# Kernel tuning notes

Hardware: AMD Instinct MI355X
Metric: run time of the kernel (lower is better)

## Reference

```python
import jax, jax.numpy as jnp
import numpy as np

EPS = 1e-8      # laplace_transform epsilon
RC = 0.5        # residual_coff
L = 2           # num_layers
NU, NB, NI, D = 100000, 30000, 50000, 128
E_UB, E_UI, E_BI = 300000, 500000, 500000


def _l2norm(x):
    # F.normalize(x, p=2, dim=1)
    n = jnp.linalg.norm(x, axis=1, keepdims=True)
    return x / jnp.maximum(n, 1e-12)


def _spmm(rows, cols, vals, feats, n):
    # sparse (COO) matmul: out[r] += vals[e] * feats[cols[e]]
    return jax.ops.segment_sum(vals[:, None] * feats[cols], rows, num_segments=n)


def _sym_norm_graph(u, v, na, nb):
    # bipartite block matrix [[0, B],[B^T, 0]] with D^-1/2 A D^-1/2 normalization
    rows = jnp.concatenate([u, v + na])
    cols = jnp.concatenate([v + na, u])
    deg = jax.ops.segment_sum(jnp.ones(rows.shape[0], jnp.float32), rows,
                              num_segments=na + nb)
    dinv = 1.0 / (jnp.sqrt(deg) + EPS)
    vals = dinv[rows] * dinv[cols]
    return rows, cols, vals


def _one_propagate(rows, cols, vals, afeat, bfeat):
    n = afeat.shape[0] + bfeat.shape[0]
    feats = jnp.concatenate([afeat, bfeat], axis=0)
    ini = _l2norm(feats)
    acc = feats  # all_feats starts with raw feats, summed at the end
    for i in range(L):
        feats = _spmm(rows, cols, vals, feats, n)
        feats = (feats + RC * ini) / (i + 2)
        feats = _l2norm(feats)
        acc = acc + feats
    return acc[:afeat.shape[0]], acc[afeat.shape[0]:]


def setup_inputs() -> dict:
    key = jax.random.key(0)
    ks = jax.random.split(key, 10)
    return {
        "users_feat": jax.random.normal(ks[0], (NU, D), jnp.float32) * 0.1,
        "bundles_feat": jax.random.normal(ks[1], (NB, D), jnp.float32) * 0.1,
        "items_feat": jax.random.normal(ks[2], (NI, D), jnp.float32) * 0.1,
        "bi_vals": jax.random.uniform(ks[3], (E_BI,), jnp.float32),
        "ub_u": jax.random.randint(ks[4], (E_UB,), 0, NU),
        "ub_b": jax.random.randint(ks[5], (E_UB,), 0, NB),
        "ui_u": jax.random.randint(ks[6], (E_UI,), 0, NU),
        "ui_i": jax.random.randint(ks[7], (E_UI,), 0, NI),
        "bi_b": jax.random.randint(ks[8], (E_BI,), 0, NB),
        "bi_i": jax.random.randint(ks[9], (E_BI,), 0, NI),
    }


def reference(users_feat, bundles_feat, items_feat, bi_vals,
              ub_u, ub_b, ui_u, ui_i, bi_b, bi_i):
    nu, nb, ni = users_feat.shape[0], bundles_feat.shape[0], items_feat.shape[0]
    # UB (history) propagation
    r, c, v = _sym_norm_graph(ub_u, ub_b, nu, nb)
    hist_users, hist_bundles = _one_propagate(r, c, v, users_feat, bundles_feat)
    # UI (affinity) propagation
    r, c, v = _sym_norm_graph(ui_u, ui_i, nu, ni)
    aff_users, ui_items = _one_propagate(r, c, v, users_feat, items_feat)
    # BI aggregation: bundles x items sparse graph @ item features
    aff_bundles = _spmm(bi_b, bi_i, bi_vals, ui_items, nb)
    # concat [aff_users, hist_users, aff_bundles, hist_bundles] along rows
    return jnp.concatenate([aff_users, hist_users, aff_bundles, hist_bundles], axis=0)
```

## Files before the change

kernel.cpp:

```cpp
#include <hip/hip_runtime.h>

#define FD   128
#define FDH  64
#define EPSN 1e-8f
#define RCC  0.5f
#define SCAN_TPB 256
#define SCAN_ELEMS 1024

typedef unsigned int uint;

__device__ __forceinline__ float wave_sum(float x) {
#pragma unroll
    for (int off = 32; off > 0; off >>= 1) x += __shfl_xor(x, off);
    return x;
}

__device__ __forceinline__ uint packbf2(float a, float b) {
    uint ua = __float_as_uint(a); ua += 0x7fffu + ((ua >> 16) & 1u);
    uint ub = __float_as_uint(b); ub += 0x7fffu + ((ub >> 16) & 1u);
    return (ua >> 16) | (ub & 0xffff0000u);
}
__device__ __forceinline__ float2 unpackbf2(uint v) {
    return make_float2(__uint_as_float(v << 16), __uint_as_float(v & 0xffff0000u));
}

__global__ void passA(const int* __restrict__ ub_u, const int* __restrict__ ub_b,
                      const int* __restrict__ ui_u, const int* __restrict__ ui_i,
                      const int* __restrict__ bi_b, const int* __restrict__ bi_i,
                      const float* __restrict__ uf, const float* __restrict__ bf,
                      const float* __restrict__ itf,
                      int E_UB, int E_UI, int E_BI, int NU, int NB, int n1, int n2, int NT,
                      int nblk_edges,
                      int* __restrict__ head, int2* __restrict__ pairLL,
                      uint* __restrict__ fini16, float* __restrict__ normf) {
    if ((int)blockIdx.x < nblk_edges) {
        int e = blockIdx.x * blockDim.x + threadIdx.x;
        if (e < E_UB) {
            int a = ub_u[e], b = ub_b[e] + NU;
            int s0 = 2 * e;
            int p0 = atomicExch(&head[a], s0);
            int p1 = atomicExch(&head[b], s0 + 1);
            ((int4*)pairLL)[e] = make_int4(p0, b, p1, a);
        } else if (e < E_UB + E_UI) {
            int f = e - E_UB;
            int a = ui_u[f], bl = ui_i[f] + NU;
            int s0 = 2 * E_UB + 2 * f;
            int p0 = atomicExch(&head[n1 + a], s0);
            int p1 = atomicExch(&head[n1 + bl], s0 + 1);
            ((int4*)pairLL)[E_UB + f] = make_int4(p0, bl, p1, a);
        } else if (e < E_UB + E_UI + E_BI) {
            int g = e - E_UB - E_UI;
            int s = 2 * E_UB + 2 * E_UI + g;
            int p = atomicExch(&head[n1 + n2 + bi_b[g]], s);
            pairLL[s] = make_int2(p, bi_i[g]);
        }
    } else {
        int w = (((int)blockIdx.x - nblk_edges) * blockDim.x + threadIdx.x) >> 6;
        int lane = threadIdx.x & 63;
        if (w >= NT) return;
        const float* src = (w < NU) ? uf + (size_t)w * FD
                         : (w < NU + NB) ? bf + (size_t)(w - NU) * FD
                         : itf + (size_t)(w - NU - NB) * FD;
        float2 x = ((const float2*)src)[lane];
        float ss = wave_sum(x.x * x.x + x.y * x.y);
        float nrm = sqrtf(ss);
        float inv = 1.0f / fmaxf(nrm, 1e-12f);
        fini16[(size_t)w * FDH + lane] = packbf2(x.x * inv, x.y * inv);
        if (lane == 0) normf[w] = nrm;
    }
}

__global__ void passB(const int* __restrict__ head, const int2* __restrict__ pairLL,
                      int NN, int n1, int n2, int NU, int NB,
                      const float* __restrict__ normf,
                      int* __restrict__ deg, float* __restrict__ dinv,
                      float* __restrict__ scaled1) {
    int r = blockIdx.x * blockDim.x + threadIdx.x;
    if (r > NN) return;
    if (r == NN) { deg[NN] = 0; return; }
    int c = 0;
    int s = head[r];
    while (s >= 0) { c++; s = pairLL[s].x; }
    deg[r] = c;
    int n12 = n1 + n2;
    if (r < n12) {
        float dv = 1.0f / (sqrtf((float)c) + EPSN);
        dinv[r] = dv;
        int node = (r < n1) ? r : ((r - n1 < NU) ? (r - n1) : (r - n1 + NB));
        scaled1[r] = dv * normf[node];
    }
}

__global__ void scan_a(const int* __restrict__ in, int* __restrict__ out,
                       int* __restrict__ bsum, int nelem) {
    __shared__ int tsum[SCAN_TPB];
    int tid = threadIdx.x;
    int base = blockIdx.x * SCAN_ELEMS + tid * 4;
    int v0 = (base + 0 < nelem) ? in[base + 0] : 0;
    int v1 = (base + 1 < nelem) ? in[base + 1] : 0;
    int v2 = (base + 2 < nelem) ? in[base + 2] : 0;
    int v3 = (base + 3 < nelem) ? in[base + 3] : 0;
    int s = v0 + v1 + v2 + v3;
    tsum[tid] = s;
    __syncthreads();
    for (int off = 1; off < SCAN_TPB; off <<= 1) {
        int y = (tid >= off) ? tsum[tid - off] : 0;
        __syncthreads();
        tsum[tid] += y;
        __syncthreads();
    }
    int excl = tsum[tid] - s;
    if (tid == SCAN_TPB - 1) bsum[blockIdx.x] = tsum[SCAN_TPB - 1];
    if (base + 0 < nelem) out[base + 0] = excl;
    excl += v0;
    if (base + 1 < nelem) out[base + 1] = excl;
    excl += v1;
    if (base + 2 < nelem) out[base + 2] = excl;
    excl += v2;
    if (base + 3 < nelem) out[base + 3] = excl;
}

__global__ void scan_b(int* __restrict__ bsum, int nb) {
    __shared__ int sm[512];
    int tid = threadIdx.x;
    int v = (tid < nb) ? bsum[tid] : 0;
    sm[tid] = v;
    __syncthreads();
    for (int off = 1; off < 512; off <<= 1) {
        int y = (tid >= off) ? sm[tid - off] : 0;
        __syncthreads();
        sm[tid] += y;
        __syncthreads();
    }
    if (tid < nb) bsum[tid] = sm[tid] - v;
}

__global__ void scan_c(int* __restrict__ out, const int* __restrict__ bsum, int nelem) {
    int base = blockIdx.x * SCAN_ELEMS + threadIdx.x * 4;
    int add = bsum[blockIdx.x];
#pragma unroll
    for (int k = 0; k < 4; ++k)
        if (base + k < nelem) out[base + k] += add;
}

__global__ void passC(const int* __restrict__ head, const int2* __restrict__ pairLL,
                      const int* __restrict__ rowptr, const float* __restrict__ bi_vals,
                      int NN, int n12, int S1,
                      int* __restrict__ cols, float* __restrict__ wts) {
    int r = blockIdx.x * blockDim.x + threadIdx.x;
    if (r >= NN) return;
    int pos = rowptr[r];
    int s = head[r];
    if (r < n12) {
        while (s >= 0) { int2 p = pairLL[s]; cols[pos++] = p.y; s = p.x; }
    } else {
        while (s >= 0) {
            int2 p = pairLL[s];
            cols[pos] = p.y;
            wts[pos - S1] = bi_vals[s - S1];
            pos++; s = p.x;
        }
    }
}

__global__ void spmm_L1(const int* __restrict__ rowptr, const int* __restrict__ cols,
                        const float* __restrict__ dinv, const float* __restrict__ scaled1,
                        const float* __restrict__ normf, const uint* __restrict__ fini16,
                        uint* __restrict__ facc16, uint* __restrict__ fX16,
                        int n1, int NU, int NB, int n12) {
    int w = (blockIdx.x * blockDim.x + threadIdx.x) >> 6;
    int lane = threadIdx.x & 63;
    if (w >= n12) return;
    int s = rowptr[w], e = rowptr[w + 1];
    bool ui = (w >= n1);
    int sB = ui ? n1 : 0;
    int nAdd = ui ? NB : 0;
    int node = ui ? ((w - n1 < NU) ? (w - n1) : (w - n1 + NB)) : w;
    float dr = dinv[w];
    float ax = 0.0f, ay = 0.0f;
    int j = s;
    for (; j + 4 <= e; j += 4) {
        int c0 = cols[j], c1 = cols[j + 1], c2 = cols[j + 2], c3 = cols[j + 3];
        float w0 = scaled1[sB + c0], w1 = scaled1[sB + c1];
        float w2 = scaled1[sB + c2], w3 = scaled1[sB + c3];
        int m0 = c0 + ((c0 >= NU) ? nAdd : 0);
        int m1 = c1 + ((c1 >= NU) ? nAdd : 0);
        int m2 = c2 + ((c2 >= NU) ? nAdd : 0);
        int m3 = c3 + ((c3 >= NU) ? nAdd : 0);
        uint x0 = fini16[(size_t)m0 * FDH + lane];
        uint x1 = fini16[(size_t)m1 * FDH + lane];
        uint x2 = fini16[(size_t)m2 * FDH + lane];
        uint x3 = fini16[(size_t)m3 * FDH + lane];
        float2 f0 = unpackbf2(x0), f1 = unpackbf2(x1);
        float2 f2 = unpackbf2(x2), f3 = unpackbf2(x3);
        ax = fmaf(w0, f0.x, ax); ay = fmaf(w0, f0.y, ay);
        ax = fmaf(w1, f1.x, ax); ay = fmaf(w1, f1.y, ay);
        ax = fmaf(w2, f2.x, ax); ay = fmaf(w2, f2.y, ay);
        ax = fmaf(w3, f3.x, ax); ay = fmaf(w3, f3.y, ay);
    }
    for (; j < e; ++j) {
        int c0 = cols[j];
        float w0 = scaled1[sB + c0];
        int m0 = c0 + ((c0 >= NU) ? nAdd : 0);
        float2 f0 = unpackbf2(fini16[(size_t)m0 * FDH + lane]);
        ax = fmaf(w0, f0.x, ax); ay = fmaf(w0, f0.y, ay);
    }
    float2 i0 = unpackbf2(fini16[(size_t)node * FDH + lane]);
    float vx = (dr * ax + RCC * i0.x) * 0.5f;
    float vy = (dr * ay + RCC * i0.y) * 0.5f;
    float ss = wave_sum(vx * vx + vy * vy);
    float inv = 1.0f / fmaxf(sqrtf(ss), 1e-12f);
    vx *= inv; vy *= inv;
    float nr = normf[node];
    facc16[(size_t)w * FDH + lane] = packbf2(fmaf(i0.x, nr, vx), fmaf(i0.y, nr, vy));
    fX16[(size_t)w * FDH + lane] = packbf2(vx * dr, vy * dr);
}

__global__ void spmm_L2(const int* __restrict__ rowptr, const int* __restrict__ cols,
                        const float* __restrict__ dinv, const uint* __restrict__ fini16,
                        const uint* __restrict__ facc16, const uint* __restrict__ fX16,
                        uint* __restrict__ items16, float* __restrict__ outp,
                        int n1, int NU, int NB, int n12) {
    int w = (blockIdx.x * blockDim.x + threadIdx.x) >> 6;
    int lane = threadIdx.x & 63;
    if (w >= n12) return;
    int s = rowptr[w], e = rowptr[w + 1];
    bool ui = (w >= n1);
    int sB = ui ? n1 : 0;
    int node = ui ? ((w - n1 < NU) ? (w - n1) : (w - n1 + NB)) : w;
    float dr = dinv[w];
    float ax = 0.0f, ay = 0.0f;
    int j = s;
    for (; j + 4 <= e; j += 4) {
        int c0 = cols[j], c1 = cols[j + 1], c2 = cols[j + 2], c3 = cols[j + 3];
        uint x0 = fX16[(size_t)(sB + c0) * FDH + lane];
        uint x1 = fX16[(size_t)(sB + c1) * FDH + lane];
        uint x2 = fX16[(size_t)(sB + c2) * FDH + lane];
        uint x3 = fX16[(size_t)(sB + c3) * FDH + lane];
        float2 f0 = unpackbf2(x0), f1 = unpackbf2(x1);
        float2 f2 = unpackbf2(x2), f3 = unpackbf2(x3);
        ax += f0.x + f1.x + f2.x + f3.x;
        ay += f0.y + f1.y + f2.y + f3.y;
    }
    for (; j < e; ++j) {
        float2 f0 = unpackbf2(fX16[(size_t)(sB + cols[j]) * FDH + lane]);
        ax += f0.x; ay += f0.y;
    }
    float2 i0 = unpackbf2(fini16[(size_t)node * FDH + lane]);
    float vx = (dr * ax + RCC * i0.x) * (1.0f / 3.0f);
    float vy = (dr * ay + RCC * i0.y) * (1.0f / 3.0f);
    float ss = wave_sum(vx * vx + vy * vy);
    float inv = 1.0f / fmaxf(sqrtf(ss), 1e-12f);
    vx *= inv; vy *= inv;
    float2 a0 = unpackbf2(facc16[(size_t)w * FDH + lane]);
    float anx = a0.x + vx, any = a0.y + vy;
    if (!ui) {
        size_t dst = (w < NU) ? (size_t)(NU + w) : (size_t)(2 * NU + NB + (w - NU));
        ((float2*)(outp + dst * FD))[lane] = make_float2(anx, any);
    } else {
        int l = w - n1;
        if (l < NU) ((float2*)(outp + (size_t)l * FD))[lane] = make_float2(anx, any);
        else        items16[(size_t)(l - NU) * FDH + lane] = packbf2(anx, any);
    }
}

__global__ void bi_gather(const int* __restrict__ rowptr, const int* __restrict__ cols,
                          const float* __restrict__ wts, int S1,
                          const uint* __restrict__ items16,
                          float* __restrict__ outb, int nb) {
    int w = (blockIdx.x * blockDim.x + threadIdx.x) >> 6;
    int lane = threadIdx.x & 63;
    if (w >= nb) return;
    int s = rowptr[w], e = rowptr[w + 1];
    float ax = 0.0f, ay = 0.0f;
    int j = s;
    for (; j + 4 <= e; j += 4) {
        int c0 = cols[j], c1 = cols[j + 1], c2 = cols[j + 2], c3 = cols[j + 3];
        float w0 = wts[j - S1], w1 = wts[j + 1 - S1];
        float w2 = wts[j + 2 - S1], w3 = wts[j + 3 - S1];
        uint x0 = items16[(size_t)c0 * FDH + lane];
        uint x1 = items16[(size_t)c1 * FDH + lane];
        uint x2 = items16[(size_t)c2 * FDH + lane];
        uint x3 = items16[(size_t)c3 * FDH + lane];
        float2 f0 = unpackbf2(x0), f1 = unpackbf2(x1);
        float2 f2 = unpackbf2(x2), f3 = unpackbf2(x3);
        ax = fmaf(w0, f0.x, ax); ay = fmaf(w0, f0.y, ay);
        ax = fmaf(w1, f1.x, ax); ay = fmaf(w1, f1.y, ay);
        ax = fmaf(w2, f2.x, ax); ay = fmaf(w2, f2.y, ay);
        ax = fmaf(w3, f3.x, ax); ay = fmaf(w3, f3.y, ay);
    }
    for (; j < e; ++j) {
        float w0 = wts[j - S1];
        float2 f0 = unpackbf2(items16[(size_t)cols[j] * FDH + lane]);
        ax = fmaf(w0, f0.x, ax); ay = fmaf(w0, f0.y, ay);
    }
    ((float2*)(outb + (size_t)w * FD))[lane] = make_float2(ax, ay);
}

extern "C" void kernel_launch(void* const* d_in, const int* in_sizes, int n_in,
                              void* d_out, int out_size, void* d_ws, size_t ws_size,
                              hipStream_t stream) {
    const float* users   = (const float*)d_in[0];
    const float* bundles = (const float*)d_in[1];
    const float* items   = (const float*)d_in[2];
    const float* bi_vals = (const float*)d_in[3];
    const int* ub_u = (const int*)d_in[4];
    const int* ub_b = (const int*)d_in[5];
    const int* ui_u = (const int*)d_in[6];
    const int* ui_i = (const int*)d_in[7];
    const int* bi_b = (const int*)d_in[8];
    const int* bi_i = (const int*)d_in[9];

    const int NU = in_sizes[0] / FD;
    const int NB = in_sizes[1] / FD;
    const int NI = in_sizes[2] / FD;
    const int E_BI = in_sizes[3];
    const int E_UB = in_sizes[4];
    const int E_UI = in_sizes[6];
    float* out = (float*)d_out;

    const int n1 = NU + NB, n2 = NU + NI;
    const int n12 = n1 + n2;
    const int NT = NU + NB + NI;
    const int NN = n12 + NB;
    const int S1 = 2 * E_UB + 2 * E_UI;
    const int TOT = S1 + E_BI;
    const int ETOT = E_UB + E_UI + E_BI;

    uint* fini16   = (uint*)d_ws;
    uint* facc16   = fini16 + (size_t)NT * FDH;
    uint* fX16     = facc16 + (size_t)n12 * FDH;
    uint* items16  = fX16 + (size_t)n12 * FDH;
    float* normf   = (float*)(items16 + (size_t)NI * FDH);
    float* dinv    = normf + NT;
    float* scaled1 = dinv + n12;
    float* wts     = scaled1 + n12;
    int* deg       = (int*)(wts + E_BI);
    int* rowptr    = deg + (NN + 1);
    int* head      = rowptr + (NN + 1);
    int* bsum      = head + NN;
    int* cols      = bsum + 512;
    int2* pairLL   = (int2*)((((size_t)(cols + TOT)) + 15) & ~(size_t)15);

    dim3 blk(256);
    auto rows_grid = [](int n) { return dim3((unsigned)((n + 3) / 4)); };
    auto thr_grid  = [](int n) { return dim3((unsigned)((n + 255) / 256)); };

    hipMemsetAsync(head, 0xFF, (size_t)NN * 4, stream);
    int nblk_edges = (ETOT + 255) / 256;
    int nblk_prep  = (NT + 3) / 4;
    passA<<<dim3((unsigned)(nblk_edges + nblk_prep)), blk, 0, stream>>>(
        ub_u, ub_b, ui_u, ui_i, bi_b, bi_i, users, bundles, items,
        E_UB, E_UI, E_BI, NU, NB, n1, n2, NT, nblk_edges,
        head, pairLL, fini16, normf);
    passB<<<thr_grid(NN + 1), blk, 0, stream>>>(head, pairLL, NN, n1, n2, NU, NB,
                                                normf, deg, dinv, scaled1);
    {
        int nelem = NN + 1;
        int nblk = (nelem + SCAN_ELEMS - 1) / SCAN_ELEMS;
        scan_a<<<dim3((unsigned)nblk), dim3(SCAN_TPB), 0, stream>>>(deg, rowptr, bsum, nelem);
        scan_b<<<dim3(1), dim3(512), 0, stream>>>(bsum, nblk);
        scan_c<<<dim3((unsigned)nblk), dim3(SCAN_TPB), 0, stream>>>(rowptr, bsum, nelem);
    }
    passC<<<thr_grid(NN), blk, 0, stream>>>(head, pairLL, rowptr, bi_vals,
                                            NN, n12, S1, cols, wts);

    spmm_L1<<<rows_grid(n12), blk, 0, stream>>>(rowptr, cols, dinv, scaled1, normf,
                                                fini16, facc16, fX16, n1, NU, NB, n12);
    spmm_L2<<<rows_grid(n12), blk, 0, stream>>>(rowptr, cols, dinv, fini16,
                                                facc16, fX16, items16, out, n1, NU, NB, n12);
    bi_gather<<<rows_grid(NB), blk, 0, stream>>>(rowptr + n12, cols, wts, S1, items16,
        out + (size_t)2 * NU * FD, NB);
}
```

Baseline: 721.7 us.

## Gather FP8 pre-scaled feature tables in both SpMM layers

Adds a conversion kernel that builds a per-graph-row FP8 table of initial features already multiplied by dinv and the original norm. Layer 1 then gathers from this table with plain adds, dropping the per-edge scale loads and index remapping. The layer-2 intermediate is also stored as FP8 instead of BF16. Together these halve the bytes moved per gathered edge, at the cost of an extra kernel pass and much lower precision (e4m3-style FP8), which risks accuracy tolerance failures.

```diff
diff --git a/kernel.cpp b/kernel.cpp
--- a/kernel.cpp
+++ b/kernel.cpp
@@ -8,6 +8,8 @@
 #define SCAN_ELEMS 1024
 
 typedef unsigned int uint;
+typedef unsigned short u16;
+typedef float fx2 __attribute__((ext_vector_type(2)));
 
 __device__ __forceinline__ float wave_sum(float x) {
 #pragma unroll
@@ -22,6 +24,12 @@
 }
 __device__ __forceinline__ float2 unpackbf2(uint v) {
     return make_float2(__uint_as_float(v << 16), __uint_as_float(v & 0xffff0000u));
+}
+__device__ __forceinline__ fx2 unpackfp8(uint v) {
+    return __builtin_amdgcn_cvt_pk_f32_fp8((int)v, false);
+}
+__device__ __forceinline__ u16 packfp8(float a, float b) {
+    return (u16)__builtin_amdgcn_cvt_pk_fp8_f32(a, b, 0, false);
 }
 
 __global__ void passA(const int* __restrict__ ub_u, const int* __restrict__ ub_b,
@@ -71,10 +79,7 @@
 }
 
 __global__ void passB(const int* __restrict__ head, const int2* __restrict__ pairLL,
-                      int NN, int n1, int n2, int NU, int NB,
-                      const float* __restrict__ normf,
-                      int* __restrict__ deg, float* __restrict__ dinv,
-                      float* __restrict__ scaled1) {
+                      int NN, int n12, int* __restrict__ deg, float* __restrict__ dinv) {
     int r = blockIdx.x * blockDim.x + threadIdx.x;
     if (r > NN) return;
     if (r == NN) { deg[NN] = 0; return; }
@@ -82,13 +87,19 @@
     int s = head[r];
     while (s >= 0) { c++; s = pairLL[s].x; }
     deg[r] = c;
-    int n12 = n1 + n2;
-    if (r < n12) {
-        float dv = 1.0f / (sqrtf((float)c) + EPSN);
-        dinv[r] = dv;
-        int node = (r < n1) ? r : ((r - n1 < NU) ? (r - n1) : (r - n1 + NB));
-        scaled1[r] = dv * normf[node];
-    }
+    if (r < n12) dinv[r] = 1.0f / (sqrtf((float)c) + EPSN);
+}
+
+__global__ void conv_g8(const uint* __restrict__ fini16, const float* __restrict__ normf,
+                        const float* __restrict__ dinv,
+                        int n1, int NU, int NB, int n12, u16* __restrict__ g8) {
+    int w = (blockIdx.x * blockDim.x + threadIdx.x) >> 6;
+    int lane = threadIdx.x & 63;
+    if (w >= n12) return;
+    int node = (w < n1) ? w : ((w - n1 < NU) ? (w - n1) : (w - n1 + NB));
+    float sc = dinv[w] * normf[node];
+    float2 f = unpackbf2(fini16[(size_t)node * FDH + lane]);
+    g8[(size_t)w * FDH + lane] = packfp8(f.x * sc, f.y * sc);
 }
 
 __global__ void scan_a(const int* __restrict__ in, int* __restrict__ out,
@@ -164,9 +175,9 @@
 }
 
 __global__ void spmm_L1(const int* __restrict__ rowptr, const int* __restrict__ cols,
-                        const float* __restrict__ dinv, const float* __restrict__ scaled1,
-                        const float* __restrict__ normf, const uint* __restrict__ fini16,
-                        uint* __restrict__ facc16, uint* __restrict__ fX16,
+                        const float* __restrict__ dinv, const float* __restrict__ normf,
+                        const uint* __restrict__ fini16, const u16* __restrict__ g8,
+                        uint* __restrict__ facc16, u16* __restrict__ fX8,
                         int n1, int NU, int NB, int n12) {
     int w = (blockIdx.x * blockDim.x + threadIdx.x) >> 6;
     int lane = threadIdx.x & 63;
@@ -174,36 +185,25 @@
     int s = rowptr[w], e = rowptr[w + 1];
     bool ui = (w >= n1);
     int sB = ui ? n1 : 0;
-    int nAdd = ui ? NB : 0;
     int node = ui ? ((w - n1 < NU) ? (w - n1) : (w - n1 + NB)) : w;
     float dr = dinv[w];
+    const u16* tab = g8 + (size_t)sB * FDH + lane;
     float ax = 0.0f, ay = 0.0f;
     int j = s;
     for (; j + 4 <= e; j += 4) {
         int c0 = cols[j], c1 = cols[j + 1], c2 = cols[j + 2], c3 = cols[j + 3];
-        float w0 = scaled1[sB + c0], w1 = scaled1[sB + c1];
-        float w2 = scaled1[sB + c2], w3 = scaled1[sB + c3];
-        int m0 = c0 + ((c0 >= NU) ? nAdd : 0);
-        int m1 = c1 + ((c1 >= NU) ? nAdd : 0);
-        int m2 = c2 + ((c2 >= NU) ? nAdd : 0);
-        int m3 = c3 + ((c3 >= NU) ? nAdd : 0);
-        uint x0 = fini16[(size_t)m0 * FDH + lane];
-        uint x1 = fini16[(size_t)m1 * FDH + lane];
-        uint x2 = fini16[(size_t)m2 * FDH + lane];
-        uint x3 = fini16[(size_t)m3 * FDH + lane];
-        float2 f0 = unpackbf2(x0), f1 = unpackbf2(x1);
-        float2 f2 = unpackbf2(x2), f3 = unpackbf2(x3);
-        ax = fmaf(w0, f0.x, ax); ay = fmaf(w0, f0.y, ay);
-        ax = fmaf(w1, f1.x, ax); ay = fmaf(w1, f1.y, ay);
-        ax = fmaf(w2, f2.x, ax); ay = fmaf(w2, f2.y, ay);
-        ax = fmaf(w3, f3.x, ax); ay = fmaf(w3, f3.y, ay);
+        uint x0 = tab[(size_t)c0 * FDH];
+        uint x1 = tab[(size_t)c1 * FDH];
+        uint x2 = tab[(size_t)c2 * FDH];
+        uint x3 = tab[(size_t)c3 * FDH];
+        fx2 f0 = unpackfp8(x0), f1 = unpackfp8(x1);
+        fx2 f2 = unpackfp8(x2), f3 = unpackfp8(x3);
+        ax += f0.x + f1.x + f2.x + f3.x;
+        ay += f0.y + f1.y + f2.y + f3.y;
     }
     for (; j < e; ++j) {
-        int c0 = cols[j];
-        float w0 = scaled1[sB + c0];
-        int m0 = c0 + ((c0 >= NU) ? nAdd : 0);
-        float2 f0 = unpackbf2(fini16[(size_t)m0 * FDH + lane]);
-        ax = fmaf(w0, f0.x, ax); ay = fmaf(w0, f0.y, ay);
+        fx2 f0 = unpackfp8(tab[(size_t)cols[j] * FDH]);
+        ax += f0.x; ay += f0.y;
     }
     float2 i0 = unpackbf2(fini16[(size_t)node * FDH + lane]);
     float vx = (dr * ax + RCC * i0.x) * 0.5f;
@@ -213,12 +213,12 @@
     vx *= inv; vy *= inv;
     float nr = normf[node];
     facc16[(size_t)w * FDH + lane] = packbf2(fmaf(i0.x, nr, vx), fmaf(i0.y, nr, vy));
-    fX16[(size_t)w * FDH + lane] = packbf2(vx * dr, vy * dr);
+    fX8[(size_t)w * FDH + lane] = packfp8(vx * dr, vy * dr);
 }
 
 __global__ void spmm_L2(const int* __restrict__ rowptr, const int* __restrict__ cols,
                         const float* __restrict__ dinv, const uint* __restrict__ fini16,
-                        const uint* __restrict__ facc16, const uint* __restrict__ fX16,
+                        const uint* __restrict__ facc16, const u16* __restrict__ fX8,
                         uint* __restrict__ items16, float* __restrict__ outp,
                         int n1, int NU, int NB, int n12) {
     int w = (blockIdx.x * blockDim.x + threadIdx.x) >> 6;
@@ -229,21 +229,22 @@
     int sB = ui ? n1 : 0;
     int node = ui ? ((w - n1 < NU) ? (w - n1) : (w - n1 + NB)) : w;
     float dr = dinv[w];
+    const u16* tab = fX8 + (size_t)sB * FDH + lane;
     float ax = 0.0f, ay = 0.0f;
     int j = s;
     for (; j + 4 <= e; j += 4) {
         int c0 = cols[j], c1 = cols[j + 1], c2 = cols[j + 2], c3 = cols[j + 3];
-        uint x0 = fX16[(size_t)(sB + c0) * FDH + lane];
-        uint x1 = fX16[(size_t)(sB + c1) * FDH + lane];
-        uint x2 = fX16[(size_t)(sB + c2) * FDH + lane];
-        uint x3 = fX16[(size_t)(sB + c3) * FDH + lane];
-        float2 f0 = unpackbf2(x0), f1 = unpackbf2(x1);
-        float2 f2 = unpackbf2(x2), f3 = unpackbf2(x3);
+        uint x0 = tab[(size_t)c0 * FDH];
+        uint x1 = tab[(size_t)c1 * FDH];
+        uint x2 = tab[(size_t)c2 * FDH];
+        uint x3 = tab[(size_t)c3 * FDH];
+        fx2 f0 = unpackfp8(x0), f1 = unpackfp8(x1);
+        fx2 f2 = unpackfp8(x2), f3 = unpackfp8(x3);
         ax += f0.x + f1.x + f2.x + f3.x;
         ay += f0.y + f1.y + f2.y + f3.y;
     }
     for (; j < e; ++j) {
-        float2 f0 = unpackbf2(fX16[(size_t)(sB + cols[j]) * FDH + lane]);
+        fx2 f0 = unpackfp8(tab[(size_t)cols[j] * FDH]);
         ax += f0.x; ay += f0.y;
     }
     float2 i0 = unpackbf2(fini16[(size_t)node * FDH + lane]);
@@ -329,12 +330,12 @@
 
     uint* fini16   = (uint*)d_ws;
     uint* facc16   = fini16 + (size_t)NT * FDH;
-    uint* fX16     = facc16 + (size_t)n12 * FDH;
-    uint* items16  = fX16 + (size_t)n12 * FDH;
-    float* normf   = (float*)(items16 + (size_t)NI * FDH);
+    uint* items16  = facc16 + (size_t)n12 * FDH;
+    u16* g8        = (u16*)(items16 + (size_t)NI * FDH);
+    u16* fX8       = g8 + (size_t)n12 * FDH;
+    float* normf   = (float*)(fX8 + (size_t)n12 * FDH);
     float* dinv    = normf + NT;
-    float* scaled1 = dinv + n12;
-    float* wts     = scaled1 + n12;
+    float* wts     = dinv + n12;
     int* deg       = (int*)(wts + E_BI);
     int* rowptr    = deg + (NN + 1);
     int* head      = rowptr + (NN + 1);
@@ -353,8 +354,8 @@
         ub_u, ub_b, ui_u, ui_i, bi_b, bi_i, users, bundles, items,
         E_UB, E_UI, E_BI, NU, NB, n1, n2, NT, nblk_edges,
         head, pairLL, fini16, normf);
-    passB<<<thr_grid(NN + 1), blk, 0, stream>>>(head, pairLL, NN, n1, n2, NU, NB,
-                                                normf, deg, dinv, scaled1);
+    passB<<<thr_grid(NN + 1), blk, 0, stream>>>(head, pairLL, NN, n12, deg, dinv);
+    conv_g8<<<rows_grid(n12), blk, 0, stream>>>(fini16, normf, dinv, n1, NU, NB, n12, g8);
     {
         int nelem = NN + 1;
         int nblk = (nelem + SCAN_ELEMS - 1) / SCAN_ELEMS;
@@ -365,10 +366,10 @@
     passC<<<thr_grid(NN), blk, 0, stream>>>(head, pairLL, rowptr, bi_vals,
                                             NN, n12, S1, cols, wts);
 
-    spmm_L1<<<rows_grid(n12), blk, 0, stream>>>(rowptr, cols, dinv, scaled1, normf,
-                                                fini16, facc16, fX16, n1, NU, NB, n12);
+    spmm_L1<<<rows_grid(n12), blk, 0, stream>>>(rowptr, cols, dinv, normf,
+                                                fini16, g8, facc16, fX8, n1, NU, NB, n12);
     spmm_L2<<<rows_grid(n12), blk, 0, stream>>>(rowptr, cols, dinv, fini16,
-                                                facc16, fX16, items16, out, n1, NU, NB, n12);
+                                                facc16, fX8, items16, out, n1, NU, NB, n12);
     bi_gather<<<rows_grid(NB), blk, 0, stream>>>(rowptr + n12, cols, wts, S1, items16,
         out + (size_t)2 * NU * FD, NB);
 }
```

Result: no change. 724.7 us (+0.4%).
